# Kernel optimization log

Measured on AMD Instinct MI355X. Metric: run time of the kernel, lower is better.

Reference implementation:

```python
import jax, jax.numpy as jnp
import numpy as np

DEPTH = 6; HEADS = 6; DIM = 384; HD = DIM // HEADS
WS = 14; WINDOW_BLOCKS = (0, 1, 3, 4)
IMG = 512; PATCH = 16; GRID = IMG // PATCH        # 32x32 token grid
PRE_GRID = 14                                      # 224 // 16 pretrain grid
SCALE = HD ** -0.5


def layer_norm(x, w, b, eps=1e-5):
    u = x.mean(-1, keepdims=True)
    s = ((x - u) ** 2).mean(-1, keepdims=True)
    return (x - u) / jnp.sqrt(s + eps) * w + b


def get_rel_pos(size, rel_pos):
    # q_size == k_size here; relative coords in [0, 2*size-2]
    coords = jnp.arange(size)[:, None] - jnp.arange(size)[None, :] + (size - 1)
    return rel_pos[coords]  # (size, size, HD)


def attention(x, qkv_w, qkv_b, proj_w, proj_b, rel_h, rel_w):
    B, H, W, C = x.shape
    N = H * W
    qkv = (x.reshape(B, N, C) @ qkv_w.T + qkv_b).reshape(B, N, 3, HEADS, HD)
    qkv = jnp.moveaxis(qkv, 2, 0).transpose(0, 1, 3, 2, 4)  # (3,B,h,N,d)
    q, k, v = qkv[0], qkv[1], qkv[2]
    attn = jnp.einsum('bhqd,bhkd->bhqk', q * SCALE, k)
    # decomposed relative position bias (ViTDet add_decomposed_rel_pos)
    Rh = get_rel_pos(H, rel_h)  # (H,H,d)
    Rw = get_rel_pos(W, rel_w)  # (W,W,d)
    rq = q.reshape(B, HEADS, H, W, HD)
    bias_h = jnp.einsum('bnhwc,hkc->bnhwk', rq, Rh)  # (B,h,H,W,H)
    bias_w = jnp.einsum('bnhwc,wkc->bnhwk', rq, Rw)  # (B,h,H,W,W)
    attn = (attn.reshape(B, HEADS, H, W, H, W)
            + bias_h[..., :, None] + bias_w[..., None, :]).reshape(B, HEADS, N, N)
    attn = jax.nn.softmax(attn, axis=-1)
    out = jnp.einsum('bhqk,bhkd->bhqd', attn, v)
    out = out.transpose(0, 2, 1, 3).reshape(B, H, W, C)
    return out @ proj_w.T + proj_b


def window_partition(x, ws):
    B, H, W, C = x.shape
    pad_h = (ws - H % ws) % ws
    pad_w = (ws - W % ws) % ws
    x = jnp.pad(x, ((0, 0), (0, pad_h), (0, pad_w), (0, 0)))
    Hp, Wp = H + pad_h, W + pad_w
    x = x.reshape(B, Hp // ws, ws, Wp // ws, ws, C)
    x = x.transpose(0, 1, 3, 2, 4, 5).reshape(-1, ws, ws, C)
    return x, Hp, Wp


def window_unpartition(win, ws, Hp, Wp, H, W):
    B = win.shape[0] // ((Hp // ws) * (Wp // ws))
    x = win.reshape(B, Hp // ws, Wp // ws, ws, ws, -1)
    x = x.transpose(0, 1, 3, 2, 4, 5).reshape(B, Hp, Wp, -1)
    return x[:, :H, :W]


def block(x, p, windowed):
    shortcut = x
    x = layer_norm(x, p['n1w'], p['n1b'])
    if windowed:
        H, W = x.shape[1], x.shape[2]
        x, Hp, Wp = window_partition(x, WS)
    x = attention(x, p['qw'], p['qb'], p['pw'], p['pb'], p['rh'], p['rw'])
    if windowed:
        x = window_unpartition(x, WS, Hp, Wp, H, W)
    x = shortcut + x
    h = layer_norm(x, p['n2w'], p['n2b'])
    h = jax.nn.gelu(h @ p['f1w'].T + p['f1b'], approximate=False)
    return x + h @ p['f2w'].T + p['f2b']


def vit_forward(x, patch_w, patch_b, pos_embed, norm1_w, norm1_b, qkv_w, qkv_b,
                proj_w, proj_b, norm2_w, norm2_b, fc1_w, fc1_b, fc2_w, fc2_b,
                rel_pos_h, rel_pos_w):
    y = jax.lax.conv_general_dilated(
        x, patch_w, (PATCH, PATCH), 'VALID',
        dimension_numbers=('NCHW', 'OIHW', 'NCHW'))
    y = y.transpose(0, 2, 3, 1) + patch_b  # (B, GRID, GRID, DIM)
    # abs pos embed: bicubic resize from pretrain 14x14 grid to 32x32
    pos = pos_embed.reshape(1, PRE_GRID, PRE_GRID, DIM)
    pos = jax.image.resize(pos, (1, GRID, GRID, DIM), 'bicubic')
    y = y + pos
    for i in range(DEPTH):
        windowed = i in WINDOW_BLOCKS
        L = 2 * WS - 1 if windowed else 2 * GRID - 1
        p = dict(n1w=norm1_w[i], n1b=norm1_b[i], qw=qkv_w[i], qb=qkv_b[i],
                 pw=proj_w[i], pb=proj_b[i], rh=rel_pos_h[i, :L], rw=rel_pos_w[i, :L],
                 n2w=norm2_w[i], n2b=norm2_b[i], f1w=fc1_w[i], f1b=fc1_b[i],
                 f2w=fc2_w[i], f2b=fc2_b[i])
        y = block(y, p, windowed)
    return y.transpose(0, 3, 1, 2)  # (B, DIM, GRID, GRID) 'last_feat'


def setup_inputs() -> dict:
    key = jax.random.key(0)
    ks = jax.random.split(key, 10)
    B = 4
    std = 0.02
    f32 = jnp.float32
    return {
        'x': jax.random.normal(ks[0], (B, 3, IMG, IMG), f32),
        'patch_w': jax.random.normal(ks[1], (DIM, 3, PATCH, PATCH), f32) * 0.05,
        'patch_b': jnp.zeros((DIM,), f32),
        'pos_embed': jax.random.normal(ks[2], (1, PRE_GRID * PRE_GRID, DIM), f32) * std,
        'norm1_w': jnp.ones((DEPTH, DIM), f32),
        'norm1_b': jnp.zeros((DEPTH, DIM), f32),
        'qkv_w': jax.random.normal(ks[3], (DEPTH, 3 * DIM, DIM), f32) * std,
        'qkv_b': jnp.zeros((DEPTH, 3 * DIM), f32),
        'proj_w': jax.random.normal(ks[4], (DEPTH, DIM, DIM), f32) * std,
        'proj_b': jnp.zeros((DEPTH, DIM), f32),
        'norm2_w': jnp.ones((DEPTH, DIM), f32),
        'norm2_b': jnp.zeros((DEPTH, DIM), f32),
        'fc1_w': jax.random.normal(ks[5], (DEPTH, 4 * DIM, DIM), f32) * std,
        'fc1_b': jnp.zeros((DEPTH, 4 * DIM), f32),
        'fc2_w': jax.random.normal(ks[6], (DEPTH, DIM, 4 * DIM), f32) * std,
        'fc2_b': jnp.zeros((DEPTH, DIM), f32),
        'rel_pos_h': jax.random.normal(ks[7], (DEPTH, 2 * GRID - 1, HD), f32) * std,
        'rel_pos_w': jax.random.normal(ks[8], (DEPTH, 2 * GRID - 1, HD), f32) * std,
    }


def reference(x, patch_w, patch_b, pos_embed, norm1_w, norm1_b, qkv_w, qkv_b,
              proj_w, proj_b, norm2_w, norm2_b, fc1_w, fc1_b, fc2_w, fc2_b,
              rel_pos_h, rel_pos_w):
    return vit_forward(x, patch_w, patch_b, pos_embed, norm1_w, norm1_b, qkv_w, qkv_b,
                       proj_w, proj_b, norm2_w, norm2_b, fc1_w, fc1_b, fc2_w, fc2_b,
                       rel_pos_h, rel_pos_w)
```

## Files before the change

### kernel.cpp

```cpp
#include <hip/hip_runtime.h>
#include <hip/hip_bf16.h>
#include <math.h>

#define B_SZ 4
#define DIM 384
#define HEADS 6
#define HD 64
#define NTOK 4096
#define WS 14
#define NWIN 36
#define WTOK 196

typedef unsigned short u16;
typedef __bf16 bf16_t;
typedef bf16_t bf16x8 __attribute__((ext_vector_type(8)));
typedef float f32x4 __attribute__((ext_vector_type(4)));

__device__ __forceinline__ float bf2f(unsigned u) { return __uint_as_float(u << 16); }
__device__ __forceinline__ u16 f2bf(float f) {
    unsigned u = __float_as_uint(f);
    unsigned r = (u + 0x7fffu + ((u >> 16) & 1u)) >> 16;
    return (u16)r;
}
__device__ __forceinline__ unsigned pk2bf(float a, float b) {
    __hip_bfloat162 h = __float22bfloat162_rn(make_float2(a, b));
    unsigned r; __builtin_memcpy(&r, &h, 4); return r;
}

__device__ __forceinline__ void ldsload16(const u16* g, u16* l) {
    __builtin_amdgcn_global_load_lds(
        (const __attribute__((address_space(1))) unsigned int*)g,
        (__attribute__((address_space(3))) unsigned int*)l, 16, 0, 0);
}

__device__ __forceinline__ int swz(int r) { return (r ^ (r >> 2)) & 3; }

__device__ inline float cubic_keys(float x) {
    x = fabsf(x);
    if (x <= 1.f) return ((1.5f * x - 2.5f) * x) * x + 1.f;
    if (x < 2.f)  return ((-0.5f * x + 2.5f) * x - 4.f) * x + 2.f;
    return 0.f;
}

__global__ __launch_bounds__(256) void setup_kernel(
        const float* __restrict__ p0, const float* __restrict__ p1,
        const float* __restrict__ p2, const float* __restrict__ p3,
        const float* __restrict__ p4, const float* __restrict__ p5,
        u16* __restrict__ wb, const float* __restrict__ pe,
        float* __restrict__ posr, const float* __restrict__ x,
        u16* __restrict__ col) {
    int i = (blockIdx.x * 256 + threadIdx.x) * 4;
    if (i < 10918656) {
        const float* s; int off;
        if      (i <   294912) { s = p0; off = 0; }
        else if (i <  2949120) { s = p1; off = 294912; }
        else if (i <  3833856) { s = p2; off = 2949120; }
        else if (i <  7372800) { s = p3; off = 3833856; }
        else if (i < 10911744) { s = p4; off = 7372800; }
        else                   { s = p5; off = 10911744; }
        float4 v = *(const float4*)(s + (i - off));
        u16 o[4] = { f2bf(v.x), f2bf(v.y), f2bf(v.z), f2bf(v.w) };
        *(uint2*)(wb + i) = *(const uint2*)o;
        return;
    }
    i -= 10918656;
    if (i < 393216) {
        int c = i % 384;
        int g = i / 384;
        int gy = g / 32, gx = g % 32;
        float wy[14], wx[14];
        float sy = (gy + 0.5f) * (14.f / 32.f) - 0.5f;
        float sx = (gx + 0.5f) * (14.f / 32.f) - 0.5f;
        float toty = 0.f, totx = 0.f;
        #pragma unroll
        for (int k = 0; k < 14; ++k) {
            wy[k] = cubic_keys(sy - (float)k); toty += wy[k];
            wx[k] = cubic_keys(sx - (float)k); totx += wx[k];
        }
        float4 acc = {0.f, 0.f, 0.f, 0.f};
        #pragma unroll 1
        for (int iy = 0; iy < 14; ++iy) {
            if (wy[iy] == 0.f) continue;
            float4 row = {0.f, 0.f, 0.f, 0.f};
            for (int ix = 0; ix < 14; ++ix) {
                if (wx[ix] == 0.f) continue;
                float4 pv = *(const float4*)(pe + (iy * 14 + ix) * 384 + c);
                row.x += wx[ix] * pv.x; row.y += wx[ix] * pv.y;
                row.z += wx[ix] * pv.z; row.w += wx[ix] * pv.w;
            }
            acc.x += wy[iy] * row.x; acc.y += wy[iy] * row.y;
            acc.z += wy[iy] * row.z; acc.w += wy[iy] * row.w;
        }
        float inv = 1.f / (toty * totx);
        acc.x *= inv; acc.y *= inv; acc.z *= inv; acc.w *= inv;
        *(float4*)(posr + i) = acc;
        return;
    }
    i -= 393216;
    if (i < 3145728) {
        int kk = i % 768;
        int p  = i / 768;
        int b  = p / 1024;
        int ph = (p % 1024) / 32;
        int pw = p % 32;
        int c = kk / 256;
        int r = kk % 256;
        int ii = r / 16, j = r % 16;
        float4 v = *(const float4*)(x + (size_t)b * 3 * 512 * 512 +
                                    (size_t)c * 512 * 512 +
                                    (size_t)(ph * 16 + ii) * 512 + (pw * 16 + j));
        u16 o[4] = { f2bf(v.x), f2bf(v.y), f2bf(v.z), f2bf(v.w) };
        *(uint2*)(col + i) = *(const uint2*)o;
    }
}

__global__ __launch_bounds__(256) void ln_kernel(const float* __restrict__ y,
        const float* __restrict__ lw, const float* __restrict__ lb,
        u16* __restrict__ lnout)
{
    int tok = blockIdx.x * 4 + (threadIdx.x >> 6);
    int t = threadIdx.x & 63;
    size_t base = (size_t)tok * 384;
    float v[6];
    float s = 0.f;
    #pragma unroll
    for (int i = 0; i < 6; ++i) {
        v[i] = y[base + t + 64 * i]; s += v[i];
    }
    #pragma unroll
    for (int off = 32; off > 0; off >>= 1) s += __shfl_xor(s, off);
    float mean = s * (1.f / 384.f);
    float vs = 0.f;
    #pragma unroll
    for (int i = 0; i < 6; ++i) { float d = v[i] - mean; vs += d * d; }
    #pragma unroll
    for (int off = 32; off > 0; off >>= 1) vs += __shfl_xor(vs, off);
    float inv = rsqrtf(vs * (1.f / 384.f) + 1e-5f);
    u16* orow = lnout + base;
    #pragma unroll
    for (int i = 0; i < 6; ++i) {
        int c = t + 64 * i;
        orow[c] = f2bf((v[i] - mean) * inv * lw[c] + lb[c]);
    }
}

__global__ __launch_bounds__(256) void out_transpose(const float* __restrict__ y,
        float* __restrict__ outT)
{
    __shared__ float T[64][65];
    int c0 = blockIdx.x * 64, m0 = blockIdx.y * 64;
    int t = threadIdx.x;
    int cl = t & 63, wv = t >> 6;
    #pragma unroll
    for (int r = 0; r < 16; ++r) {
        int ml = wv * 16 + r;
        T[ml][cl] = y[(size_t)(m0 + ml) * 384 + c0 + cl];
    }
    __syncthreads();
    int b = m0 >> 10, g0 = m0 & 1023;
    int gl = t & 63;
    #pragma unroll
    for (int r = 0; r < 16; ++r) {
        int ccl = wv * 16 + r;
        outT[((size_t)(b * 384 + c0 + ccl)) * 1024 + g0 + gl] = T[gl][ccl];
    }
}

__global__ __launch_bounds__(256) void mfma_gemm4(
        const u16* __restrict__ A, const u16* __restrict__ Wt,
        const float* __restrict__ bias,
        u16* __restrict__ outb,
        int M, int N, int K, int act)
{
    __shared__ u16 As[2][8192];
    __shared__ u16 Bs[2][4096];
    int t = threadIdx.x;
    int lane = t & 63, wave = t >> 6;
    int wm = (wave >> 1) * 64, wn = (wave & 1) * 32;
    int m0 = blockIdx.y * 128, n0 = blockIdx.x * 64;

    int r0 = t >> 2,        c0 = ((t & 3) ^ swz(t >> 2)) * 8;
    int r1 = 64 + (t >> 2), c1 = ((t & 3) ^ swz(64 + (t >> 2))) * 8;
    const u16* a0 = A + (size_t)(m0 + r0) * K + c0;
    const u16* a1 = A + (size_t)(m0 + r1) * K + c1;
    const u16* b0 = Wt + (size_t)(n0 + r0) * K + c0;

    auto stage = [&](int k0, int buf) {
        ldsload16(a0 + k0,      &As[buf][wave * 512]);
        ldsload16(a1 + k0,      &As[buf][2048 + wave * 512]);
        ldsload16(b0 + k0,      &Bs[buf][wave * 512]);
        ldsload16(a0 + k0 + 32, &As[buf][4096 + wave * 512]);
        ldsload16(a1 + k0 + 32, &As[buf][6144 + wave * 512]);
        ldsload16(b0 + k0 + 32, &Bs[buf][2048 + wave * 512]);
    };

    f32x4 acc[4][2] = {};
    int row_a = wm + (lane & 15);
    int row_b = wn + (lane & 15);
    int lq = lane >> 4;
    int nchunks = K / 64;

    stage(0, 0);
    __syncthreads();

    for (int ci = 0; ci < nchunks; ++ci) {
        int p = ci & 1;
        bool pref = (ci + 1 < nchunks);
        if (pref) stage((ci + 1) * 64, 1 - p);
        #pragma unroll
        for (int hf = 0; hf < 2; ++hf) {
            bf16x8 af[4], bfr[2];
            #pragma unroll
            for (int i = 0; i < 4; ++i) {
                int r = row_a + i * 16;
                af[i] = *(const bf16x8*)&As[p][hf * 4096 + r * 32 + ((lq ^ swz(r)) * 8)];
            }
            #pragma unroll
            for (int j = 0; j < 2; ++j) {
                int r = row_b + j * 16;
                bfr[j] = *(const bf16x8*)&Bs[p][hf * 2048 + r * 32 + ((lq ^ swz(r)) * 8)];
            }
            #pragma unroll
            for (int i = 0; i < 4; ++i)
                #pragma unroll
                for (int j = 0; j < 2; ++j)
                    acc[i][j] = __builtin_amdgcn_mfma_f32_16x16x32_bf16(
                        af[i], bfr[j], acc[i][j], 0, 0, 0);
        }
        if (pref) __syncthreads();
    }

    int colq = lane & 15, rowq = (lane >> 4) * 4;
    #pragma unroll
    for (int i = 0; i < 4; ++i) {
        #pragma unroll
        for (int rr = 0; rr < 4; ++rr) {
            int m = m0 + wm + i * 16 + rowq + rr;
            size_t mo = (size_t)m * N;
            #pragma unroll
            for (int j = 0; j < 2; ++j) {
                int n = n0 + wn + j * 16 + colq;
                float v = acc[i][j][rr] + bias[n];
                if (act)  v = 0.5f * v * (1.f + erff(v * 0.70710678118654752f));
                outb[mo + n] = f2bf(v);
            }
        }
    }
}

__global__ __launch_bounds__(256) void mfma_gemm64(
        const u16* __restrict__ A, const u16* __restrict__ Wt,
        const float* __restrict__ bias, const float* __restrict__ posr,
        float* __restrict__ y, int addy, int M, int N, int K)
{
    __shared__ u16 As[2][4096];
    __shared__ u16 Bs[2][4096];
    int t = threadIdx.x;
    int lane = t & 63, wave = t >> 6;
    int wm = (wave >> 1) * 32, wn = (wave & 1) * 32;
    int m0 = blockIdx.y * 64, n0 = blockIdx.x * 64;

    int r0 = t >> 2, c0 = ((t & 3) ^ swz(t >> 2)) * 8;
    const u16* a0 = A + (size_t)(m0 + r0) * K + c0;
    const u16* b0 = Wt + (size_t)(n0 + r0) * K + c0;

    auto stage = [&](int k0, int buf) {
        ldsload16(a0 + k0,      &As[buf][wave * 512]);
        ldsload16(b0 + k0,      &Bs[buf][wave * 512]);
        ldsload16(a0 + k0 + 32, &As[buf][2048 + wave * 512]);
        ldsload16(b0 + k0 + 32, &Bs[buf][2048 + wave * 512]);
    };

    f32x4 acc[2][2] = {};
    int row_a = wm + (lane & 15);
    int row_b = wn + (lane & 15);
    int lq = lane >> 4;
    int nchunks = K / 64;

    stage(0, 0);
    __syncthreads();

    for (int ci = 0; ci < nchunks; ++ci) {
        int p = ci & 1;
        bool pref = (ci + 1 < nchunks);
        if (pref) stage((ci + 1) * 64, 1 - p);
        #pragma unroll
        for (int hf = 0; hf < 2; ++hf) {
            bf16x8 af[2], bfr[2];
            #pragma unroll
            for (int i = 0; i < 2; ++i) {
                int r = row_a + i * 16;
                af[i] = *(const bf16x8*)&As[p][hf * 2048 + r * 32 + ((lq ^ swz(r)) * 8)];
            }
            #pragma unroll
            for (int j = 0; j < 2; ++j) {
                int r = row_b + j * 16;
                bfr[j] = *(const bf16x8*)&Bs[p][hf * 2048 + r * 32 + ((lq ^ swz(r)) * 8)];
            }
            #pragma unroll
            for (int i = 0; i < 2; ++i)
                #pragma unroll
                for (int j = 0; j < 2; ++j)
                    acc[i][j] = __builtin_amdgcn_mfma_f32_16x16x32_bf16(
                        af[i], bfr[j], acc[i][j], 0, 0, 0);
        }
        if (pref) __syncthreads();
    }

    int colq = lane & 15, rowq = (lane >> 4) * 4;
    #pragma unroll
    for (int i = 0; i < 2; ++i) {
        #pragma unroll
        for (int rr = 0; rr < 4; ++rr) {
            int m = m0 + wm + i * 16 + rowq + rr;
            size_t mo = (size_t)m * N;
            #pragma unroll
            for (int j = 0; j < 2; ++j) {
                int n = n0 + wn + j * 16 + colq;
                float v = acc[i][j][rr] + bias[n];
                if (posr) v += posr[(size_t)(m & 1023) * 384 + n];
                if (addy) v += y[mo + n];
                y[mo + n] = v;
            }
        }
    }
}

template<int N, int W>
__global__ __launch_bounds__(256) void attn_mfma(const u16* __restrict__ qkv,
        const u16* __restrict__ qkb, const float* __restrict__ rh,
        const float* __restrict__ rw, u16* __restrict__ outb,
        float* __restrict__ opart, float* __restrict__ lpart)
{
    constexpr int JS = (W == 32) ? 64 : 32;
    constexpr int L  = (W == 32) ? 63 : 27;
    constexpr int CTR = W - 1;
    constexpr int KSPAN = (W == 32) ? 512 : 224;
    constexpr int NKT = KSPAN / 32;
    __shared__ u16 KV[11776];
    __shared__ u16 bhl[64 * 66];
    __shared__ u16 bwl[64 * 66];
    __shared__ u16 Qt[64 * 66];

    u16* Pb = KV + 9216;
    u16* Rt = KV;

    int t = threadIdx.x, lane = t & 63, wave = t >> 6;
    int quad = lane >> 4, l15 = lane & 15;
    int uh = blockIdx.x, qb0 = blockIdx.y * 64;
    int z = (W == 32) ? blockIdx.z : 0;
    int kstart = z * KSPAN;
    int h = uh % HEADS, u = uh / HEADS;
    size_t tbase = (size_t)u * 1024;
    int wb_ = u / 9, wr = u - wb_ * 9;
    int wy = wr / 3, wx = wr - wy * 3;

    auto tok14 = [&](int iy, int ix) -> const u16* {
        int gy = wy * WS + iy, gx = wx * WS + ix;
        if (gy < 32 && gx < 32)
            return qkv + (size_t)(wb_ * 1024 + gy * 32 + gx) * 1152;
        return qkb;
    };
    auto rowptr = [&](int lq2) -> const u16* {
        if constexpr (W == 32) {
            return qkv + (tbase + lq2) * 1152;
        } else {
            int iy = lq2 / WS, ix = lq2 - iy * WS;
            return tok14(iy, ix);
        }
    };

    {
        int q = t & 63, ch0 = (t >> 6) * 16;
        int qc = qb0 + q; if (qc >= N) qc = N - 1;
        const u16* qp = rowptr(qc) + h * 64 + ch0;
        uint4 a = *(const uint4*)qp;
        uint4 b = *(const uint4*)(qp + 8);
        u16 vals[16];
        *(uint4*)vals = a; *(uint4*)(vals + 8) = b;
        #pragma unroll
        for (int c = 0; c < 16; ++c)
            Qt[(ch0 + c) * 66 + q] = ((qb0 + q) < N) ? vals[c] : (u16)0;
    }

    #pragma unroll
    for (int table = 0; table < 2; ++table) {
        __syncthreads();
        const float* tab = table ? rw : rh;
        for (int idx = t; idx < JS * 8; idx += 256) {
            int j = idx >> 3, cc0 = (idx & 7) * 8;
            u16 tmp[8];
            if (j < L) {
                const float* src = tab + (size_t)j * 64 + cc0;
                #pragma unroll
                for (int c = 0; c < 8; ++c) tmp[c] = f2bf(src[c]);
            } else {
                #pragma unroll
                for (int c = 0; c < 8; ++c) tmp[c] = 0;
            }
            *(uint4*)&Rt[j * 72 + cc0] = *(uint4*)tmp;
        }
        __syncthreads();
        if (wave < JS / 16) {
            int jt = wave;
            bf16x8 af0 = *(const bf16x8*)&Rt[(jt * 16 + l15) * 72 + quad * 8];
            bf16x8 af1 = *(const bf16x8*)&Rt[(jt * 16 + l15) * 72 + 32 + quad * 8];
            u16* dst = table ? bwl : bhl;
            #pragma unroll
            for (int qt = 0; qt < 4; ++qt) {
                bf16x8 qf0, qf1;
                u16* p0 = (u16*)&qf0; u16* p1 = (u16*)&qf1;
                #pragma unroll
                for (int zz = 0; zz < 8; ++zz) {
                    p0[zz] = Qt[(quad * 8 + zz) * 66 + qt * 16 + l15];
                    p1[zz] = Qt[(32 + quad * 8 + zz) * 66 + qt * 16 + l15];
                }
                f32x4 acc = {};
                acc = __builtin_amdgcn_mfma_f32_16x16x32_bf16(af0, qf0, acc, 0, 0, 0);
                acc = __builtin_amdgcn_mfma_f32_16x16x32_bf16(af1, qf1, acc, 0, 0, 0);
                #pragma unroll
                for (int r = 0; r < 4; ++r)
                    dst[(qt * 16 + l15) * 66 + jt * 16 + quad * 4 + r] = f2bf(acc[r]);
            }
        }
    }
    __syncthreads();

    int skey = (wave * 64 + lane) >> 3;
    int sc8  = ((wave * 64 + lane) & 7) ^ (skey & 7);
    int vkey = t & 31, vch0 = (t >> 5) * 8;
    int siy = 0, six = 0, viy = 0, vix = 0;
    if constexpr (W != 32) {
        int k0 = kstart + skey;
        siy = k0 / WS; six = k0 - siy * WS;
        int k1 = kstart + vkey;
        viy = k1 / WS; vix = k1 - viy * WS;
    }
    auto adv = [](int& iy, int& ix) { ix += 4; iy += 2; if (ix >= WS) { ix -= WS; ++iy; } };

    {
        const u16* kp = (W == 32) ? qkv + (tbase + kstart + skey) * 1152
                                  : tok14(siy, six);
        ldsload16(kp + 384 + h * 64 + sc8 * 8, KV + wave * 512);
        const u16* vp = (W == 32) ? qkv + (tbase + kstart + vkey) * 1152
                                  : tok14(viy, vix);
        uint4 vv = *(const uint4*)(vp + 768 + h * 64 + vch0);
        u16 tmp[8]; *(uint4*)tmp = vv;
        u16* vdst = KV + 4096;
        #pragma unroll
        for (int c = 0; c < 8; ++c) vdst[(vch0 + c) * 40 + vkey] = tmp[c];
        if constexpr (W != 32) { adv(siy, six); adv(viy, vix); }
    }

    bf16x8 qf[2];
    #pragma unroll
    for (int hc = 0; hc < 2; ++hc) {
        u16* qv = (u16*)&qf[hc];
        #pragma unroll
        for (int j = 0; j < 8; ++j)
            qv[j] = Qt[(hc * 32 + quad * 8 + j) * 66 + wave * 16 + l15];
    }
    int qme = wave * 16 + l15;
    bool wactive = (W == 32) ? true : ((qb0 + wave * 16) < N);
    int qq = qb0 + qme; if (qq >= N) qq = N - 1;
    int qh = qq / W, qw = qq - qh * W;
    float bwreg[2][4];
    int kh_[2][4], kw_[2][4];
    #pragma unroll
    for (int kc2 = 0; kc2 < 2; ++kc2)
        #pragma unroll
        for (int r = 0; r < 4; ++r) {
            int keyl = kc2 * 16 + quad * 4 + r;
            if constexpr (W == 32) {
                bwreg[kc2][r] = bf2f(bwl[qme * 66 + (qw - keyl + CTR)]);
            } else {
                kh_[kc2][r] = keyl / WS;
                kw_[kc2][r] = keyl - kh_[kc2][r] * WS;
            }
        }

    f32x4 of[4] = {};
    float lsum = 0.f;
    __syncthreads();

    for (int kt = 0; kt < NKT; ++kt) {
        int kb = kstart + kt * 32;
        int p = kt & 1;
        const u16* ksp = KV + p * 2048;
        const u16* vtp = KV + 4096 + p * 2560;
        bool pref = (kt + 1 < NKT);
        uint4 vpref;
        if (pref) {
            const u16* kp = (W == 32) ? qkv + (tbase + kb + 32 + skey) * 1152
                                      : tok14(siy, six);
            ldsload16(kp + 384 + h * 64 + sc8 * 8, KV + (1 - p) * 2048 + wave * 512);
            const u16* vp = (W == 32) ? qkv + (tbase + kb + 32 + vkey) * 1152
                                      : tok14(viy, vix);
            vpref = *(const uint4*)(vp + 768 + h * 64 + vch0);
            if constexpr (W != 32) { adv(siy, six); adv(viy, vix); }
        }

        if (wactive) {
            f32x4 st[2] = {};
            #pragma unroll
            for (int hc = 0; hc < 2; ++hc) {
                #pragma unroll
                for (int kc2 = 0; kc2 < 2; ++kc2) {
                    int key = kc2 * 16 + l15;
                    int c8 = hc * 4 + quad;
                    int pp = key * 8 + (c8 ^ (key & 7));
                    bf16x8 kf = *(const bf16x8*)&ksp[pp * 8];
                    st[kc2] = __builtin_amdgcn_mfma_f32_16x16x32_bf16(
                        kf, qf[hc], st[kc2], 0, 0, 0);
                }
            }
            float bh_t = 0.f;
            if constexpr (W == 32) bh_t = bf2f(bhl[qme * 66 + (qh - (kb >> 5) + CTR)]);
            #pragma unroll
            for (int kc2 = 0; kc2 < 2; ++kc2) {
                float pv4[4];
                #pragma unroll
                for (int r = 0; r < 4; ++r) {
                    int keyl = kc2 * 16 + quad * 4 + r;
                    float b;
                    if constexpr (W == 32) {
                        b = bh_t + bwreg[kc2][r];
                    } else {
                        b = bf2f(bhl[qme * 66 + (qh - kh_[kc2][r] + CTR)]) +
                            bf2f(bwl[qme * 66 + (qw - kw_[kc2][r] + CTR)]);
                    }
                    float pv = __expf(fmaf(st[kc2][r], 0.125f, b));
                    if (kb + keyl >= N) pv = 0.f;
                    lsum += pv;
                    pv4[r] = pv;
                }
                uint2 pk;
                pk.x = pk2bf(pv4[0], pv4[1]);
                pk.y = pk2bf(pv4[2], pv4[3]);
                *(uint2*)&Pb[wave * 640 + l15 * 40 + kc2 * 16 + quad * 4] = pk;
            }
            if constexpr (W != 32) {
                #pragma unroll
                for (int kc2 = 0; kc2 < 2; ++kc2)
                    #pragma unroll
                    for (int r = 0; r < 4; ++r) {
                        kw_[kc2][r] += 4; kh_[kc2][r] += 2;
                        if (kw_[kc2][r] >= WS) { kw_[kc2][r] -= WS; ++kh_[kc2][r]; }
                    }
            }
            bf16x8 pf = *(const bf16x8*)&Pb[wave * 640 + l15 * 40 + quad * 8];
            #pragma unroll
            for (int ca = 0; ca < 4; ++ca) {
                bf16x8 vf = *(const bf16x8*)&vtp[(ca * 16 + l15) * 40 + quad * 8];
                of[ca] = __builtin_amdgcn_mfma_f32_16x16x32_bf16(
                    vf, pf, of[ca], 0, 0, 0);
            }
        }

        if (pref) {
            u16 tmp[8]; *(uint4*)tmp = vpref;
            u16* vdst = KV + 4096 + (1 - p) * 2560;
            #pragma unroll
            for (int c = 0; c < 8; ++c) vdst[(vch0 + c) * 40 + vkey] = tmp[c];
            __syncthreads();
        }
    }

    lsum += __shfl_xor(lsum, 16);
    lsum += __shfl_xor(lsum, 32);
    int q = qb0 + qme;
    if constexpr (W == 32) {
        size_t ridx = (size_t)z * 24576 + (size_t)uh * 1024 + q;
        float* op = opart + ridx * 64;
        #pragma unroll
        for (int ca = 0; ca < 4; ++ca)
            *(float4*)&op[ca * 16 + quad * 4] = (float4){of[ca][0], of[ca][1],
                                                         of[ca][2], of[ca][3]};
        if (quad == 0) lpart[ridx] = lsum;
    } else {
        float inv = 1.f / lsum;
        if (q < N) {
            int iy = q / WS, ix = q - iy * WS;
            int gy = wy * WS + iy, gx = wx * WS + ix;
            if (gy >= 32 || gx >= 32) return;
            u16* op = outb + (size_t)(wb_ * 1024 + gy * 32 + gx) * 384 + h * 64;
            #pragma unroll
            for (int ca = 0; ca < 4; ++ca) {
                uint2 pk;
                pk.x = pk2bf(of[ca][0] * inv, of[ca][1] * inv);
                pk.y = pk2bf(of[ca][2] * inv, of[ca][3] * inv);
                *(uint2*)&op[ca * 16 + quad * 4] = pk;
            }
        }
    }
}

__global__ __launch_bounds__(256) void attn_merge_kernel(const float* __restrict__ O,
        const float* __restrict__ Lp, u16* __restrict__ attb)
{
    int t = threadIdx.x;
    int idx = blockIdx.x * 4 + (t >> 6);
    int ch = t & 63;
    float o = O[(size_t)idx * 64 + ch] + O[((size_t)24576 + idx) * 64 + ch];
    float l = Lp[idx] + Lp[24576 + idx];
    int uh = idx >> 10, q = idx & 1023;
    int u = uh / 6, h = uh - u * 6;
    attb[((size_t)(u * 1024 + q)) * 384 + h * 64 + ch] = f2bf(o / l);
}

static inline void launch_gemm(const u16* A, const u16* W, const float* bias,
                               u16* outb, int M, int N, int K, int act,
                               hipStream_t s) {
    dim3 g(N / 64, M / 128, 1);
    mfma_gemm4<<<g, 256, 0, s>>>(A, W, bias, outb, M, N, K, act);
}

static inline void launch_gemm64(const u16* A, const u16* W, const float* bias,
                                 const float* posr, float* y, int addy,
                                 int M, int N, int K, hipStream_t s) {
    dim3 g(N / 64, M / 64, 1);
    mfma_gemm64<<<g, 256, 0, s>>>(A, W, bias, posr, y, addy, M, N, K);
}

extern "C" void kernel_launch(void* const* d_in, const int* in_sizes, int n_in,
                              void* d_out, int out_size, void* d_ws, size_t ws_size,
                              hipStream_t stream) {
    const float* x      = (const float*)d_in[0];
    const float* patchw = (const float*)d_in[1];
    const float* patchb = (const float*)d_in[2];
    const float* pos    = (const float*)d_in[3];
    const float* n1w    = (const float*)d_in[4];
    const float* n1b    = (const float*)d_in[5];
    const float* qkvw   = (const float*)d_in[6];
    const float* qkvb   = (const float*)d_in[7];
    const float* pw     = (const float*)d_in[8];
    const float* pb     = (const float*)d_in[9];
    const float* n2w    = (const float*)d_in[10];
    const float* n2b    = (const float*)d_in[11];
    const float* f1w    = (const float*)d_in[12];
    const float* f1b    = (const float*)d_in[13];
    const float* f2w    = (const float*)d_in[14];
    const float* f2b    = (const float*)d_in[15];
    const float* rph    = (const float*)d_in[16];
    const float* rpw    = (const float*)d_in[17];
    float* out = (float*)d_out;

    float* y   = (float*)d_ws;
    u16* attb  = (u16*)(y + 1572864);
    u16* mlpb  = attb + 1572864;
    u16* lnb   = mlpb + 6291456;
    u16* qkvx  = lnb + 1572864;
    u16* rsrv  = qkvx + 4718592;
    u16* wb    = rsrv + 7864320;
    float* posr = (float*)(wb + 10918656);

    u16* colb  = rsrv;
    float* Opart   = (float*)mlpb;
    float* Lpart   = (float*)lnb;

    u16* wb_patch = wb;
    u16* wb_qkv   = wb + 294912;
    u16* wb_pw    = wb + 2949120;
    u16* wb_f1    = wb + 3833856;
    u16* wb_f2    = wb + 7372800;
    u16* wqb      = wb + 10911744;

    setup_kernel<<<(14457600 / 4 + 255) / 256, 256, 0, stream>>>(
        patchw, qkvw, pw, f1w, f2w, qkvb, wb, pos, posr, x, colb);

    launch_gemm64(colb, wb_patch, patchb, posr, y, 0, NTOK, 384, 768, stream);
    ln_kernel<<<1024, 256, 0, stream>>>(y, n1w, n1b, lnb);

    for (int i = 0; i < 6; ++i) {
        bool windowed = (i == 0 || i == 1 || i == 3 || i == 4);
        const float* rh = rph + (size_t)i * 63 * 64;
        const float* rw = rpw + (size_t)i * 63 * 64;
        launch_gemm(lnb, wb_qkv + (size_t)i * 442368, qkvb + i * 1152,
                    qkvx, NTOK, 1152, 384, 0, stream);
        if (windowed) {
            attn_mfma<WTOK, WS><<<dim3(NWIN * HEADS, 4, 1), 256, 0, stream>>>(
                qkvx, wqb + i * 1152, rh, rw, attb, nullptr, nullptr);
        } else {
            attn_mfma<1024, 32><<<dim3(B_SZ * HEADS, 16, 2), 256, 0, stream>>>(
                qkvx, wqb + i * 1152, rh, rw, nullptr, Opart, Lpart);
            attn_merge_kernel<<<6144, 256, 0, stream>>>(Opart, Lpart, attb);
        }
        launch_gemm64(attb, wb_pw + (size_t)i * 147456, pb + i * 384,
                      nullptr, y, 1, NTOK, 384, 384, stream);
        ln_kernel<<<1024, 256, 0, stream>>>(y, n2w + i * 384, n2b + i * 384, lnb);
        launch_gemm(lnb, wb_f1 + (size_t)i * 589824, f1b + i * 1536,
                    mlpb, NTOK, 1536, 384, 1, stream);
        launch_gemm64(mlpb, wb_f2 + (size_t)i * 589824, f2b + i * 384,
                      nullptr, y, 1, NTOK, 384, 1536, stream);
        if (i < 5)
            ln_kernel<<<1024, 256, 0, stream>>>(y, n1w + (i + 1) * 384,
                                                n1b + (i + 1) * 384, lnb);
        else
            out_transpose<<<dim3(6, 64), 256, 0, stream>>>(y, out);
    }
}
```

Measured before the change: 710.6 us.

## Narrow N=384 GEMM tiles, merge rel-pos table passes, precompute key offsets, vectorize merge

Several independent changes. The N=384 output GEMMs now use 64x32 tiles, which doubles the grid to 768 blocks so more of the GPU's compute units have work, at the cost of reloading A tiles twice as often. The attention kernel fills both rel-pos tables in one pass with a single barrier, gives the windowed case's waves one table each, and replaces per-iteration key-coordinate register updates with a precomputed shared offset table. The attention merge kernel now processes float4 per thread and writes packed bf16 pairs.

```diff
diff --git a/kernel.cpp b/kernel.cpp
--- a/kernel.cpp
+++ b/kernel.cpp
@@ -248,30 +248,32 @@
     }
 }
 
-__global__ __launch_bounds__(256) void mfma_gemm64(
+__global__ __launch_bounds__(256) void mfma_gemm32(
         const u16* __restrict__ A, const u16* __restrict__ Wt,
         const float* __restrict__ bias, const float* __restrict__ posr,
         float* __restrict__ y, int addy, int M, int N, int K)
 {
     __shared__ u16 As[2][4096];
-    __shared__ u16 Bs[2][4096];
+    __shared__ u16 Bs[2][2048];
     int t = threadIdx.x;
     int lane = t & 63, wave = t >> 6;
-    int wm = (wave >> 1) * 32, wn = (wave & 1) * 32;
-    int m0 = blockIdx.y * 64, n0 = blockIdx.x * 64;
+    int wm = (wave >> 1) * 32, wn = (wave & 1) * 16;
+    int m0 = blockIdx.y * 64, n0 = blockIdx.x * 32;
 
     int r0 = t >> 2, c0 = ((t & 3) ^ swz(t >> 2)) * 8;
     const u16* a0 = A + (size_t)(m0 + r0) * K + c0;
-    const u16* b0 = Wt + (size_t)(n0 + r0) * K + c0;
+    int tb = t & 127;
+    int rb = tb >> 2, cb = ((tb & 3) ^ swz(tb >> 2)) * 8;
+    const u16* b0 = Wt + (size_t)(n0 + rb) * K + cb;
 
     auto stage = [&](int k0, int buf) {
         ldsload16(a0 + k0,      &As[buf][wave * 512]);
-        ldsload16(b0 + k0,      &Bs[buf][wave * 512]);
         ldsload16(a0 + k0 + 32, &As[buf][2048 + wave * 512]);
-        ldsload16(b0 + k0 + 32, &Bs[buf][2048 + wave * 512]);
+        if (wave < 2) ldsload16(b0 + k0,      &Bs[buf][wave * 512]);
+        else          ldsload16(b0 + k0 + 32, &Bs[buf][1024 + (wave - 2) * 512]);
     };
 
-    f32x4 acc[2][2] = {};
+    f32x4 acc[2] = {};
     int row_a = wm + (lane & 15);
     int row_b = wn + (lane & 15);
     int lq = lane >> 4;
@@ -286,23 +288,20 @@
         if (pref) stage((ci + 1) * 64, 1 - p);
         #pragma unroll
         for (int hf = 0; hf < 2; ++hf) {
-            bf16x8 af[2], bfr[2];
+            bf16x8 af[2], bf0;
             #pragma unroll
             for (int i = 0; i < 2; ++i) {
                 int r = row_a + i * 16;
                 af[i] = *(const bf16x8*)&As[p][hf * 2048 + r * 32 + ((lq ^ swz(r)) * 8)];
             }
-            #pragma unroll
-            for (int j = 0; j < 2; ++j) {
-                int r = row_b + j * 16;
-                bfr[j] = *(const bf16x8*)&Bs[p][hf * 2048 + r * 32 + ((lq ^ swz(r)) * 8)];
+            {
+                int r = row_b;
+                bf0 = *(const bf16x8*)&Bs[p][hf * 1024 + r * 32 + ((lq ^ swz(r)) * 8)];
             }
             #pragma unroll
             for (int i = 0; i < 2; ++i)
-                #pragma unroll
-                for (int j = 0; j < 2; ++j)
-                    acc[i][j] = __builtin_amdgcn_mfma_f32_16x16x32_bf16(
-                        af[i], bfr[j], acc[i][j], 0, 0, 0);
+                acc[i] = __builtin_amdgcn_mfma_f32_16x16x32_bf16(
+                    af[i], bf0, acc[i], 0, 0, 0);
         }
         if (pref) __syncthreads();
     }
@@ -314,14 +313,11 @@
         for (int rr = 0; rr < 4; ++rr) {
             int m = m0 + wm + i * 16 + rowq + rr;
             size_t mo = (size_t)m * N;
-            #pragma unroll
-            for (int j = 0; j < 2; ++j) {
-                int n = n0 + wn + j * 16 + colq;
-                float v = acc[i][j][rr] + bias[n];
-                if (posr) v += posr[(size_t)(m & 1023) * 384 + n];
-                if (addy) v += y[mo + n];
-                y[mo + n] = v;
-            }
+            int n = n0 + wn + colq;
+            float v = acc[i][rr] + bias[n];
+            if (posr) v += posr[(size_t)(m & 1023) * 384 + n];
+            if (addy) v += y[mo + n];
+            y[mo + n] = v;
         }
     }
 }
@@ -341,6 +337,7 @@
     __shared__ u16 bhl[64 * 66];
     __shared__ u16 bwl[64 * 66];
     __shared__ u16 Qt[64 * 66];
+    __shared__ unsigned kofs[224];
 
     u16* Pb = KV + 9216;
     u16* Rt = KV;
@@ -383,28 +380,40 @@
             Qt[(ch0 + c) * 66 + q] = ((qb0 + q) < N) ? vals[c] : (u16)0;
     }
 
-    #pragma unroll
-    for (int table = 0; table < 2; ++table) {
-        __syncthreads();
+    if constexpr (W != 32) {
+        if (t < 224) {
+            int kh = t / WS;
+            kofs[t] = (unsigned)kh | ((unsigned)(t - kh * WS) << 16);
+        }
+    }
+
+    for (int idx = t; idx < JS * 16; idx += 256) {
+        int table = (idx >= JS * 8) ? 1 : 0;
+        int id2 = idx & (JS * 8 - 1);
+        int j = id2 >> 3, cc0 = (id2 & 7) * 8;
         const float* tab = table ? rw : rh;
-        for (int idx = t; idx < JS * 8; idx += 256) {
-            int j = idx >> 3, cc0 = (idx & 7) * 8;
-            u16 tmp[8];
-            if (j < L) {
-                const float* src = tab + (size_t)j * 64 + cc0;
-                #pragma unroll
-                for (int c = 0; c < 8; ++c) tmp[c] = f2bf(src[c]);
-            } else {
-                #pragma unroll
-                for (int c = 0; c < 8; ++c) tmp[c] = 0;
-            }
-            *(uint4*)&Rt[j * 72 + cc0] = *(uint4*)tmp;
-        }
-        __syncthreads();
-        if (wave < JS / 16) {
-            int jt = wave;
-            bf16x8 af0 = *(const bf16x8*)&Rt[(jt * 16 + l15) * 72 + quad * 8];
-            bf16x8 af1 = *(const bf16x8*)&Rt[(jt * 16 + l15) * 72 + 32 + quad * 8];
+        u16 tmp[8];
+        if (j < L) {
+            const float* src = tab + (size_t)j * 64 + cc0;
+            #pragma unroll
+            for (int c = 0; c < 8; ++c) tmp[c] = f2bf(src[c]);
+        } else {
+            #pragma unroll
+            for (int c = 0; c < 8; ++c) tmp[c] = 0;
+        }
+        *(uint4*)&Rt[table * JS * 72 + j * 72 + cc0] = *(uint4*)tmp;
+    }
+    __syncthreads();
+
+    {
+        int tb0 = (W == 32) ? 0 : (wave >> 1);
+        int ntb = (W == 32) ? 2 : 1;
+        int jt  = (W == 32) ? wave : (wave & 1);
+        for (int tt = 0; tt < ntb; ++tt) {
+            int table = tb0 + tt;
+            const u16* Rtt = Rt + table * JS * 72;
+            bf16x8 af0 = *(const bf16x8*)&Rtt[(jt * 16 + l15) * 72 + quad * 8];
+            bf16x8 af1 = *(const bf16x8*)&Rtt[(jt * 16 + l15) * 72 + 32 + quad * 8];
             u16* dst = table ? bwl : bhl;
             #pragma unroll
             for (int qt = 0; qt < 4; ++qt) {
@@ -464,20 +473,17 @@
     bool wactive = (W == 32) ? true : ((qb0 + wave * 16) < N);
     int qq = qb0 + qme; if (qq >= N) qq = N - 1;
     int qh = qq / W, qw = qq - qh * W;
+    int qh13 = qh + CTR, qw13 = qw + CTR;
     float bwreg[2][4];
-    int kh_[2][4], kw_[2][4];
-    #pragma unroll
-    for (int kc2 = 0; kc2 < 2; ++kc2)
-        #pragma unroll
-        for (int r = 0; r < 4; ++r) {
-            int keyl = kc2 * 16 + quad * 4 + r;
-            if constexpr (W == 32) {
+    if constexpr (W == 32) {
+        #pragma unroll
+        for (int kc2 = 0; kc2 < 2; ++kc2)
+            #pragma unroll
+            for (int r = 0; r < 4; ++r) {
+                int keyl = kc2 * 16 + quad * 4 + r;
                 bwreg[kc2][r] = bf2f(bwl[qme * 66 + (qw - keyl + CTR)]);
-            } else {
-                kh_[kc2][r] = keyl / WS;
-                kw_[kc2][r] = keyl - kh_[kc2][r] * WS;
-            }
-        }
+            }
+    }
 
     f32x4 of[4] = {};
     float lsum = 0.f;
@@ -522,15 +528,17 @@
                 #pragma unroll
                 for (int r = 0; r < 4; ++r) {
                     int keyl = kc2 * 16 + quad * 4 + r;
-                    float b;
+                    float pv;
                     if constexpr (W == 32) {
-                        b = bh_t + bwreg[kc2][r];
+                        float b = bh_t + bwreg[kc2][r];
+                        pv = __expf(fmaf(st[kc2][r], 0.125f, b));
                     } else {
-                        b = bf2f(bhl[qme * 66 + (qh - kh_[kc2][r] + CTR)]) +
-                            bf2f(bwl[qme * 66 + (qw - kw_[kc2][r] + CTR)]);
+                        unsigned ko = kofs[kb + keyl];
+                        float b = bf2f(bhl[qme * 66 + qh13 - (int)(ko & 0xffffu)]) +
+                                  bf2f(bwl[qme * 66 + qw13 - (int)(ko >> 16)]);
+                        pv = __expf(fmaf(st[kc2][r], 0.125f, b));
+                        if (kb + keyl >= N) pv = 0.f;
                     }
-                    float pv = __expf(fmaf(st[kc2][r], 0.125f, b));
-                    if (kb + keyl >= N) pv = 0.f;
                     lsum += pv;
                     pv4[r] = pv;
                 }
@@ -538,15 +546,6 @@
                 pk.x = pk2bf(pv4[0], pv4[1]);
                 pk.y = pk2bf(pv4[2], pv4[3]);
                 *(uint2*)&Pb[wave * 640 + l15 * 40 + kc2 * 16 + quad * 4] = pk;
-            }
-            if constexpr (W != 32) {
-                #pragma unroll
-                for (int kc2 = 0; kc2 < 2; ++kc2)
-                    #pragma unroll
-                    for (int r = 0; r < 4; ++r) {
-                        kw_[kc2][r] += 4; kh_[kc2][r] += 2;
-                        if (kw_[kc2][r] >= WS) { kw_[kc2][r] -= WS; ++kh_[kc2][r]; }
-                    }
             }
             bf16x8 pf = *(const bf16x8*)&Pb[wave * 640 + l15 * 40 + quad * 8];
             #pragma unroll
@@ -598,14 +597,18 @@
 __global__ __launch_bounds__(256) void attn_merge_kernel(const float* __restrict__ O,
         const float* __restrict__ Lp, u16* __restrict__ attb)
 {
-    int t = threadIdx.x;
-    int idx = blockIdx.x * 4 + (t >> 6);
-    int ch = t & 63;
-    float o = O[(size_t)idx * 64 + ch] + O[((size_t)24576 + idx) * 64 + ch];
-    float l = Lp[idx] + Lp[24576 + idx];
+    int gi = blockIdx.x * 256 + threadIdx.x;
+    int idx = gi >> 4;
+    int ch = (gi & 15) * 4;
+    float4 o0 = *(const float4*)&O[(size_t)idx * 64 + ch];
+    float4 o1 = *(const float4*)&O[((size_t)24576 + idx) * 64 + ch];
+    float inv = 1.f / (Lp[idx] + Lp[24576 + idx]);
     int uh = idx >> 10, q = idx & 1023;
     int u = uh / 6, h = uh - u * 6;
-    attb[((size_t)(u * 1024 + q)) * 384 + h * 64 + ch] = f2bf(o / l);
+    uint2 pk;
+    pk.x = pk2bf((o0.x + o1.x) * inv, (o0.y + o1.y) * inv);
+    pk.y = pk2bf((o0.z + o1.z) * inv, (o0.w + o1.w) * inv);
+    *(uint2*)(attb + ((size_t)(u * 1024 + q)) * 384 + h * 64 + ch) = pk;
 }
 
 static inline void launch_gemm(const u16* A, const u16* W, const float* bias,
@@ -615,11 +618,11 @@
     mfma_gemm4<<<g, 256, 0, s>>>(A, W, bias, outb, M, N, K, act);
 }
 
-static inline void launch_gemm64(const u16* A, const u16* W, const float* bias,
+static inline void launch_gemm32(const u16* A, const u16* W, const float* bias,
                                  const float* posr, float* y, int addy,
                                  int M, int N, int K, hipStream_t s) {
-    dim3 g(N / 64, M / 64, 1);
-    mfma_gemm64<<<g, 256, 0, s>>>(A, W, bias, posr, y, addy, M, N, K);
+    dim3 g(N / 32, M / 64, 1);
+    mfma_gemm32<<<g, 256, 0, s>>>(A, W, bias, posr, y, addy, M, N, K);
 }
 
 extern "C" void kernel_launch(void* const* d_in, const int* in_sizes, int n_in,
@@ -668,7 +671,7 @@
     setup_kernel<<<(14457600 / 4 + 255) / 256, 256, 0, stream>>>(
         patchw, qkvw, pw, f1w, f2w, qkvb, wb, pos, posr, x, colb);
 
-    launch_gemm64(colb, wb_patch, patchb, posr, y, 0, NTOK, 384, 768, stream);
+    launch_gemm32(colb, wb_patch, patchb, posr, y, 0, NTOK, 384, 768, stream);
     ln_kernel<<<1024, 256, 0, stream>>>(y, n1w, n1b, lnb);
 
     for (int i = 0; i < 6; ++i) {
@@ -683,14 +686,14 @@
         } else {
             attn_mfma<1024, 32><<<dim3(B_SZ * HEADS, 16, 2), 256, 0, stream>>>(
                 qkvx, wqb + i * 1152, rh, rw, nullptr, Opart, Lpart);
-            attn_merge_kernel<<<6144, 256, 0, stream>>>(Opart, Lpart, attb);
-        }
-        launch_gemm64(attb, wb_pw + (size_t)i * 147456, pb + i * 384,
+            attn_merge_kernel<<<1536, 256, 0, stream>>>(Opart, Lpart, attb);
+        }
+        launch_gemm32(attb, wb_pw + (size_t)i * 147456, pb + i * 384,
                       nullptr, y, 1, NTOK, 384, 384, stream);
         ln_kernel<<<1024, 256, 0, stream>>>(y, n2w + i * 384, n2b + i * 384, lnb);
         launch_gemm(lnb, wb_f1 + (size_t)i * 589824, f1b + i * 1536,
                     mlpb, NTOK, 1536, 384, 1, stream);
-        launch_gemm64(mlpb, wb_f2 + (size_t)i * 589824, f2b + i * 384,
+        launch_gemm32(mlpb, wb_f2 + (size_t)i * 589824, f2b + i * 384,
                       nullptr, y, 1, NTOK, 384, 1536, stream);
         if (i < 5)
             ln_kernel<<<1024, 256, 0, stream>>>(y, n1w + (i + 1) * 384,
```

After: 678.0 us. 1.05x faster.
